# Kernel optimization log

Measured on AMD Instinct MI355X. Metric: run time of the kernel, lower is better.

## Reference

```python
import jax, jax.numpy as jnp
import numpy as np

D = 512      # d_model
H = 8        # num_heads
DH = D // H  # d_head = 64
WIN = 10     # window_size
DFF = 2048   # d_ff
EPS = 1e-5   # LayerNorm eps


def _layernorm(x, w, b):
    mu = jnp.mean(x, axis=-1, keepdims=True)
    var = jnp.mean(jnp.square(x - mu), axis=-1, keepdims=True)
    return (x - mu) * jax.lax.rsqrt(var + EPS) * w + b


def setup_inputs() -> dict:
    key = jax.random.key(0)
    ks = jax.random.split(key, 8)
    s = 0.02
    inp = {
        "z": jax.random.normal(ks[0], (4, 2048, D), jnp.float32),
        "Wq": jax.random.normal(ks[1], (D, D), jnp.float32) * s,
        "bq": jnp.zeros((D,), jnp.float32),
        "Wk": jax.random.normal(ks[2], (D, D), jnp.float32) * s,
        "bk": jnp.zeros((D,), jnp.float32),
        "Wv": jax.random.normal(ks[3], (D, D), jnp.float32) * s,
        "bv": jnp.zeros((D,), jnp.float32),
        "Wo": jax.random.normal(ks[4], (D, D), jnp.float32) * s,
        "bo": jnp.zeros((D,), jnp.float32),
        "ln1_w": jnp.ones((D,), jnp.float32),
        "ln1_b": jnp.zeros((D,), jnp.float32),
        "W1": jax.random.normal(ks[5], (D, DFF), jnp.float32) * s,
        "b1": jnp.zeros((DFF,), jnp.float32),
        "W2": jax.random.normal(ks[6], (DFF, D), jnp.float32) * s,
        "b2": jnp.zeros((D,), jnp.float32),
        "ln2_w": jnp.ones((D,), jnp.float32),
        "ln2_b": jnp.zeros((D,), jnp.float32),
    }
    return inp


def reference(z, Wq, bq, Wk, bk, Wv, bv, Wo, bo, ln1_w, ln1_b, W1, b1, W2, b2, ln2_w, ln2_b):
    B, T, Dm = z.shape
    # projections -> [B, H, T, DH]
    q = (z @ Wq + bq).reshape(B, T, H, DH).transpose(0, 2, 1, 3)
    k = (z @ Wk + bk).reshape(B, T, H, DH).transpose(0, 2, 1, 3)
    v = (z @ Wv + bv).reshape(B, T, H, DH).transpose(0, 2, 1, 3)
    scale = 1.0 / jnp.sqrt(jnp.asarray(DH, z.dtype))
    scores = jnp.einsum('bhqd,bhkd->bhqk', q, k) * scale  # [B,H,T,T]
    idx = jnp.arange(T)
    dist = idx[:, None] - idx[None, :]
    valid = (dist >= 0) & (dist < WIN)
    neg = jnp.finfo(scores.dtype).min
    scores = jnp.where(valid[None, None], scores, neg)
    attn = jax.nn.softmax(scores, axis=-1)  # dropout is identity in eval
    out = jnp.einsum('bhqk,bhkd->bhqd', attn, v)
    out = out.transpose(0, 2, 1, 3).reshape(B, T, Dm)
    out = out @ Wo + bo
    z = _layernorm(z + out, ln1_w, ln1_b)
    # FFN with exact (erf) GELU, matching torch nn.GELU default
    ff = jax.nn.gelu(z @ W1 + b1, approximate=False) @ W2 + b2
    z = _layernorm(z + ff, ln2_w, ln2_b)
    return z
```

## Files before the change

### kernel.cpp

```cpp
#include <hip/hip_runtime.h>
#include <cstdint>
#include <cstddef>

#define DEV __device__ __forceinline__

typedef __bf16 bf16x8 __attribute__((ext_vector_type(8)));
typedef float f32x4 __attribute__((ext_vector_type(4)));
typedef unsigned short us8 __attribute__((ext_vector_type(8)));
typedef unsigned short us4 __attribute__((ext_vector_type(4)));

typedef const __attribute__((address_space(1))) unsigned int GUI;
typedef __attribute__((address_space(3))) unsigned int LUI;

DEV unsigned short f2bf(float f) {
  unsigned int u = __builtin_bit_cast(unsigned int, f);
  u += 0x7fffu + ((u >> 16) & 1u);
  return (unsigned short)(u >> 16);
}
DEV float bf2f(unsigned short h) {
  unsigned int u = ((unsigned int)h) << 16;
  return __builtin_bit_cast(float, u);
}

DEV void tr32(const float* __restrict__ in, unsigned short* __restrict__ out,
              int K, int N, int k0, int n0) {
  __shared__ float tile[32][33];
  const int tx = threadIdx.x & 31, ty = threadIdx.x >> 5;
#pragma unroll
  for (int i = 0; i < 32; i += 8)
    tile[ty + i][tx] = in[(size_t)(k0 + ty + i) * N + n0 + tx];
  __syncthreads();
#pragma unroll
  for (int i = 0; i < 32; i += 8)
    out[(size_t)(n0 + ty + i) * K + k0 + tx] = f2bf(tile[tx][ty + i]);
}

__global__ __launch_bounds__(256) void k_prep(
    const float* __restrict__ z, unsigned short* __restrict__ zb,
    const float* __restrict__ Wq, const float* __restrict__ Wk,
    const float* __restrict__ Wv, const float* __restrict__ Wo,
    unsigned short* __restrict__ Wsq,
    const float* __restrict__ W1, unsigned short* __restrict__ W1T,
    const float* __restrict__ W2, unsigned short* __restrict__ W2T,
    const float* __restrict__ bq, const float* __restrict__ bk,
    const float* __restrict__ bv, float* __restrict__ biasqkv) {
  const int j = blockIdx.x;
  const int tid = threadIdx.x;
  if (j < 4096) {
    int i = j * 256 + tid;
    float4 v = ((const float4*)z)[i];
    us4 o;
    o.x = f2bf(v.x); o.y = f2bf(v.y); o.z = f2bf(v.z); o.w = f2bf(v.w);
    *(us4*)(zb + (size_t)i * 4) = o;
  } else if (j < 5120) {
    int t = j - 4096;
    int mat = t >> 8, tile = t & 255;
    const float* in = mat == 0 ? Wq : mat == 1 ? Wk : mat == 2 ? Wv : Wo;
    tr32(in, Wsq + (size_t)mat * 262144, 512, 512, (tile >> 4) * 32, (tile & 15) * 32);
  } else if (j < 6144) {
    int t = j - 5120;
    tr32(W1, W1T, 512, 2048, (t / 64) * 32, (t % 64) * 32);
  } else if (j < 7168) {
    int t = j - 6144;
    tr32(W2, W2T, 2048, 512, (t / 16) * 32, (t % 16) * 32);
  } else {
    for (int i = tid; i < 1536; i += 256)
      biasqkv[i] = (i < 512) ? bq[i] : (i < 1024 ? bk[i - 512] : bv[i - 1024]);
  }
}

template <int MODE>
DEV void gemm_body(const unsigned short* __restrict__ A,
                   const unsigned short* __restrict__ BT,
                   const float* __restrict__ bias,
                   unsigned short* __restrict__ outp,
                   int K, int N) {
  __shared__ __align__(16) unsigned short As[2 * 8192];
  __shared__ __align__(16) unsigned short Bs[2 * 8192];
  const int tid = threadIdx.x;
  const int wave = tid >> 6, lane = tid & 63;
  const int wm = wave >> 1, wn = wave & 1;
  const int q = lane >> 4, l15 = lane & 15;

  const int nx = gridDim.x, ny = gridDim.y;
  const int nwg = nx * ny;
  const int lid = blockIdx.y * nx + blockIdx.x;
  const int q8 = nwg >> 3, r8 = nwg & 7;
  const int xcd = lid & 7, slot = lid >> 3;
  const int wid = (xcd < r8 ? xcd * (q8 + 1) : r8 * (q8 + 1) + (xcd - r8) * q8) + slot;
  const int bx = wid % nx;
  const int by = wid / nx;

  const int rbase = by * 128;
  const int nbase = bx * 128;
  const int nkt = K >> 6;

  float bv_[4];
#pragma unroll
  for (int n = 0; n < 4; ++n) bv_[n] = bias[nbase + wn * 64 + n * 16 + l15];
  asm volatile("s_waitcnt vmcnt(0)" ::: "memory");

  auto STAGE = [&](int buf, int k0) {
#pragma unroll
    for (int t = 0; t < 4; ++t) {
      int s = t * 256 + tid;
      int row = s >> 3;
      int col = ((s & 7) ^ (row & 7)) << 3;
      const unsigned short* ga = A + (size_t)(rbase + row) * K + k0 + col;
      const unsigned short* gb = BT + (size_t)(nbase + row) * K + k0 + col;
      const int dst = buf * 8192 + (t * 256 + wave * 64) * 8;
      __builtin_amdgcn_global_load_lds((GUI*)ga, (LUI*)(As + dst), 16, 0, 0);
      __builtin_amdgcn_global_load_lds((GUI*)gb, (LUI*)(Bs + dst), 16, 0, 0);
    }
  };

  f32x4 acc[4][4] = {};
  STAGE(0, 0);

  for (int kt = 0; kt < nkt; ++kt) {
    const int cur = kt & 1;
    if (kt + 1 < nkt) {
      STAGE(cur ^ 1, (kt + 1) * 64);
      asm volatile("s_waitcnt vmcnt(8)" ::: "memory");
    } else {
      asm volatile("s_waitcnt vmcnt(0)" ::: "memory");
    }
    __builtin_amdgcn_s_barrier();

#pragma unroll
    for (int ks = 0; ks < 2; ++ks) {
      bf16x8 af[4], bfr[4];
#pragma unroll
      for (int m = 0; m < 4; ++m) {
        int row = wm * 64 + m * 16 + l15;
        int ch = (ks * 4 + q) ^ (row & 7);
        af[m] = __builtin_bit_cast(bf16x8, *(const us8*)(As + cur * 8192 + row * 64 + ch * 8));
      }
#pragma unroll
      for (int n = 0; n < 4; ++n) {
        int row = wn * 64 + n * 16 + l15;
        int ch = (ks * 4 + q) ^ (row & 7);
        bfr[n] = __builtin_bit_cast(bf16x8, *(const us8*)(Bs + cur * 8192 + row * 64 + ch * 8));
      }
      __builtin_amdgcn_s_setprio(1);
#pragma unroll
      for (int m = 0; m < 4; ++m)
#pragma unroll
        for (int n = 0; n < 4; ++n)
          acc[m][n] = __builtin_amdgcn_mfma_f32_16x16x32_bf16(af[m], bfr[n], acc[m][n], 0, 0, 0);
      __builtin_amdgcn_s_setprio(0);
    }
    asm volatile("s_waitcnt lgkmcnt(0)" ::: "memory");
    __builtin_amdgcn_s_barrier();
  }

#pragma unroll
  for (int m = 0; m < 4; ++m) {
    int grow0 = rbase + wm * 64 + m * 16 + (q << 2);
#pragma unroll
    for (int n = 0; n < 4; ++n) {
      int gcol = nbase + wn * 64 + n * 16 + l15;
#pragma unroll
      for (int r = 0; r < 4; ++r) {
        float v = acc[m][n][r] + bv_[n];
        if (MODE == 2) v = 0.5f * v * (1.0f + erff(v * 0.70710678118654752f));
        outp[(size_t)(grow0 + r) * N + gcol] = f2bf(v);
      }
    }
  }
}

__global__ __launch_bounds__(256) void k_qkv(const unsigned short* __restrict__ A,
                                             const unsigned short* __restrict__ BT,
                                             const float* __restrict__ bias,
                                             unsigned short* __restrict__ outp, int K, int N) {
  gemm_body<0>(A, BT, bias, outp, K, N);
}
__global__ __launch_bounds__(256) void k_wo(const unsigned short* __restrict__ A,
                                            const unsigned short* __restrict__ BT,
                                            const float* __restrict__ bias,
                                            unsigned short* __restrict__ outp, int K, int N) {
  gemm_body<0>(A, BT, bias, outp, K, N);
}
__global__ __launch_bounds__(256) void k_ffn1(const unsigned short* __restrict__ A,
                                              const unsigned short* __restrict__ BT,
                                              const float* __restrict__ bias,
                                              unsigned short* __restrict__ outp, int K, int N) {
  gemm_body<2>(A, BT, bias, outp, K, N);
}
__global__ __launch_bounds__(256) void k_ffn2(const unsigned short* __restrict__ A,
                                              const unsigned short* __restrict__ BT,
                                              const float* __restrict__ bias,
                                              unsigned short* __restrict__ outp, int K, int N) {
  gemm_body<0>(A, BT, bias, outp, K, N);
}

__global__ __launch_bounds__(64) void k_attn(const unsigned short* __restrict__ qkv,
                                             unsigned short* __restrict__ attnb) {
  __shared__ float Qt[64 * 35];
  __shared__ float Kt[64 * 45];
  __shared__ float P[32 * 12];

  const int lane = threadIdx.x;
  const int bid = blockIdx.x;
  const int chunk = bid & 63;
  const int bh = bid >> 6;
  const int h = bh & 7, b = bh >> 3;
  const int i0 = chunk * 32;
  const int b2048 = b * 2048;
  const int h64 = h * 64;

#pragma unroll 8
  for (int r = 0; r < 41; ++r) {
    int jloc = i0 - 9 + r;
    int jc = jloc < 0 ? 0 : jloc;
    Kt[lane * 45 + r] = bf2f(qkv[(size_t)(b2048 + jc) * 1536 + 512 + h64 + lane]);
  }
#pragma unroll 8
  for (int r = 0; r < 32; ++r) {
    Qt[lane * 35 + r] = bf2f(qkv[(size_t)(b2048 + i0 + r) * 1536 + h64 + lane]);
  }
  __syncthreads();

  const int qe = lane & 31, dh = lane >> 5;
  float s[10];
#pragma unroll
  for (int jj = 0; jj < 10; ++jj) s[jj] = 0.f;
#pragma unroll
  for (int dd = 0; dd < 32; ++dd) {
    int d = dh * 32 + dd;
    float qd = Qt[d * 35 + qe];
#pragma unroll
    for (int jj = 0; jj < 10; ++jj)
      s[jj] = fmaf(qd, Kt[d * 45 + qe + jj], s[jj]);
  }
#pragma unroll
  for (int jj = 0; jj < 10; ++jj) s[jj] += __shfl_xor(s[jj], 32);

  const int iG = i0 + qe;
#pragma unroll
  for (int jj = 0; jj < 10; ++jj)
    s[jj] = (iG - 9 + jj >= 0) ? s[jj] * 0.125f : -1e30f;
  float mx = s[9];
#pragma unroll
  for (int jj = 0; jj < 9; ++jj) mx = fmaxf(mx, s[jj]);
  float den = 0.f;
#pragma unroll
  for (int jj = 0; jj < 10; ++jj) {
    s[jj] = __expf(s[jj] - mx);
    den += s[jj];
  }
  float inv = 1.f / den;
  if (lane < 32) {
#pragma unroll
    for (int jj = 0; jj < 10; ++jj) P[qe * 12 + jj] = s[jj] * inv;
  }
  __syncthreads();

  for (int q0 = 0; q0 < 32; q0 += 4) {
    float vv[13];
#pragma unroll
    for (int t = 0; t < 13; ++t) {
      int jloc = i0 + q0 - 9 + t;
      int jc = jloc < 0 ? 0 : jloc;
      vv[t] = bf2f(qkv[(size_t)(b2048 + jc) * 1536 + 1024 + h64 + lane]);
    }
#pragma unroll
    for (int qq = 0; qq < 4; ++qq) {
      const int qy = q0 + qq;
      const float* pp = &P[qy * 12];
      float o = 0.f;
#pragma unroll
      for (int jj = 0; jj < 10; ++jj) o = fmaf(pp[jj], vv[qq + jj], o);
      attnb[(size_t)(b2048 + i0 + qy) * 512 + h64 + lane] = f2bf(o);
    }
  }
}

template <int OUTF32>
DEV void ln_body(const unsigned short* __restrict__ res,
                 const unsigned short* __restrict__ add,
                 const float* __restrict__ w,
                 const float* __restrict__ bb,
                 void* __restrict__ outp) {
  const int wave = threadIdx.x >> 6, lane = threadIdx.x & 63;
  const int row = blockIdx.x * 4 + wave;
  float x[8];
  us8 r = *(const us8*)(res + (size_t)row * 512 + lane * 8);
  us8 a = *(const us8*)(add + (size_t)row * 512 + lane * 8);
  float sum = 0.f, ss = 0.f;
#pragma unroll
  for (int j = 0; j < 8; ++j) {
    x[j] = bf2f(r[j]) + bf2f(a[j]);
    sum += x[j];
    ss += x[j] * x[j];
  }
#pragma unroll
  for (int m = 32; m >= 1; m >>= 1) {
    sum += __shfl_xor(sum, m);
    ss += __shfl_xor(ss, m);
  }
  const float mu = sum * (1.f / 512.f);
  float var = ss * (1.f / 512.f) - mu * mu;
  const float rstd = rsqrtf(var + 1e-5f);
  const int c = lane * 8;
  float o[8];
#pragma unroll
  for (int j = 0; j < 8; ++j) o[j] = (x[j] - mu) * rstd * w[c + j] + bb[c + j];
  if (OUTF32 == 0) {
    us8 u;
#pragma unroll
    for (int j = 0; j < 8; ++j) u[j] = f2bf(o[j]);
    *(us8*)((unsigned short*)outp + (size_t)row * 512 + c) = u;
  } else {
    float4 u0, u1;
    u0.x = o[0]; u0.y = o[1]; u0.z = o[2]; u0.w = o[3];
    u1.x = o[4]; u1.y = o[5]; u1.z = o[6]; u1.w = o[7];
    float4* o4 = (float4*)((float*)outp + (size_t)row * 512 + c);
    o4[0] = u0; o4[1] = u1;
  }
}

__global__ __launch_bounds__(256) void k_ln_mid(const unsigned short* __restrict__ res,
                                                const unsigned short* __restrict__ add,
                                                const float* __restrict__ w,
                                                const float* __restrict__ bb,
                                                unsigned short* __restrict__ outp) {
  ln_body<0>(res, add, w, bb, outp);
}
__global__ __launch_bounds__(256) void k_ln_out(const unsigned short* __restrict__ res,
                                                const unsigned short* __restrict__ add,
                                                const float* __restrict__ w,
                                                const float* __restrict__ bb,
                                                float* __restrict__ outp) {
  ln_body<1>(res, add, w, bb, outp);
}

extern "C" void kernel_launch(void* const* d_in, const int* in_sizes, int n_in,
                              void* d_out, int out_size, void* d_ws, size_t ws_size,
                              hipStream_t stream) {
  const float* z    = (const float*)d_in[0];
  const float* Wq   = (const float*)d_in[1];
  const float* bq   = (const float*)d_in[2];
  const float* Wk   = (const float*)d_in[3];
  const float* bk   = (const float*)d_in[4];
  const float* Wv   = (const float*)d_in[5];
  const float* bv   = (const float*)d_in[6];
  const float* Wo   = (const float*)d_in[7];
  const float* bo   = (const float*)d_in[8];
  const float* ln1w = (const float*)d_in[9];
  const float* ln1b = (const float*)d_in[10];
  const float* W1   = (const float*)d_in[11];
  const float* b1   = (const float*)d_in[12];
  const float* W2   = (const float*)d_in[13];
  const float* b2   = (const float*)d_in[14];
  const float* ln2w = (const float*)d_in[15];
  const float* ln2b = (const float*)d_in[16];
  float* out = (float*)d_out;

  char* ws = (char*)d_ws;
  size_t off = 0;
  auto alloc = [&](size_t bytes) {
    char* p = ws + off;
    off += (bytes + 255) & ~(size_t)255;
    return p;
  };
  unsigned short* Wsq   = (unsigned short*)alloc((size_t)2048 * 512 * 2);
  unsigned short* WTqkv = Wsq;
  unsigned short* WoT   = Wsq + (size_t)1536 * 512;
  unsigned short* W1T   = (unsigned short*)alloc((size_t)2048 * 512 * 2);
  unsigned short* W2T   = (unsigned short*)alloc((size_t)512 * 2048 * 2);
  float*          biasqkv = (float*)alloc(1536 * 4);
  unsigned short* zb    = (unsigned short*)alloc((size_t)8192 * 512 * 2);
  unsigned short* z1b   = (unsigned short*)alloc((size_t)8192 * 512 * 2);
  unsigned short* qkvb  = (unsigned short*)alloc((size_t)8192 * 1536 * 2);
  unsigned short* attnb = (unsigned short*)alloc((size_t)8192 * 512 * 2);
  unsigned short* woout = (unsigned short*)alloc((size_t)8192 * 512 * 2);
  unsigned short* f2out = (unsigned short*)alloc((size_t)8192 * 512 * 2);
  unsigned short* ff    = qkvb;

  k_prep<<<7169, 256, 0, stream>>>(z, zb, Wq, Wk, Wv, Wo, Wsq, W1, W1T, W2, W2T,
                                   bq, bk, bv, biasqkv);
  k_qkv<<<dim3(12, 64), 256, 0, stream>>>(zb, WTqkv, biasqkv, qkvb, 512, 1536);
  k_attn<<<2048, 64, 0, stream>>>(qkvb, attnb);
  k_wo<<<dim3(4, 64), 256, 0, stream>>>(attnb, WoT, bo, woout, 512, 512);
  k_ln_mid<<<2048, 256, 0, stream>>>(zb, woout, ln1w, ln1b, z1b);
  k_ffn1<<<dim3(16, 64), 256, 0, stream>>>(z1b, W1T, b1, ff, 512, 2048);
  k_ffn2<<<dim3(4, 64), 256, 0, stream>>>(ff, W2T, b2, f2out, 2048, 512);
  k_ln_out<<<2048, 256, 0, stream>>>(z1b, f2out, ln2w, ln2b, out);
}
```

Baseline: 147.7 us.

## Use 256x256 GEMM tiles with split-K partials reduced in LayerNorm

Adds a 512-thread GEMM with 256x256 output tiles and double-buffered LDS staging, used for the Wo, FFN1 and FFN2 projections. The Wo and FFN2 GEMMs are split four ways along K, each writing a bf16 partial plane, and the following LayerNorm kernels sum the four planes with the residual. The larger tiles raise operand reuse per workgroup, and split-K keeps enough workgroups in flight for the narrow N=512 outputs. In exchange it writes and reads extra partial-sum traffic, rounds each partial to bf16, and uses 128 KB of LDS per workgroup.

```diff
diff --git a/kernel.cpp b/kernel.cpp
--- a/kernel.cpp
+++ b/kernel.cpp
@@ -69,12 +69,120 @@
   }
 }
 
+template <int MODE, int SPLITK>
+DEV void gemm256_body(const unsigned short* __restrict__ A,
+                      const unsigned short* __restrict__ BT,
+                      const float* __restrict__ bias,
+                      unsigned short* __restrict__ outp,
+                      int K, int N) {
+  __shared__ __align__(16) unsigned short As[2 * 16384];
+  __shared__ __align__(16) unsigned short Bs[2 * 16384];
+  const int tid = threadIdx.x;
+  const int wave = tid >> 6, lane = tid & 63;
+  const int wm = wave >> 2, wn = wave & 3;
+
+  const int nx = gridDim.x, ny = gridDim.y;
+  const int nwg = nx * ny * SPLITK;
+  const int lid = (blockIdx.z * ny + blockIdx.y) * nx + blockIdx.x;
+  const int q8 = nwg >> 3, r8 = nwg & 7;
+  const int xcd = lid & 7, slot = lid >> 3;
+  const int wid = (xcd < r8 ? xcd * (q8 + 1) : r8 * (q8 + 1) + (xcd - r8) * q8) + slot;
+  const int nbz = nx * SPLITK;
+  const int bxz = wid % nbz;
+  const int by  = wid / nbz;
+  const int bx  = bxz % nx;
+  const int z   = bxz / nx;
+
+  const int rbase = by * 256;
+  const int nbase = bx * 256;
+  const int nkt = (K / SPLITK) >> 6;
+  const int kb = z * (K / SPLITK);
+
+  float bv_[4];
+#pragma unroll
+  for (int n = 0; n < 4; ++n) {
+    int gcol = nbase + wn * 64 + n * 16 + (lane & 15);
+    bv_[n] = (z == 0) ? bias[gcol] : 0.f;
+  }
+  asm volatile("s_waitcnt vmcnt(0)" ::: "memory");
+
+  auto STAGE = [&](int buf, int k0) {
+#pragma unroll
+    for (int t = 0; t < 4; ++t) {
+      int s = t * 512 + tid;
+      int row = s >> 3;
+      int col = ((s & 7) ^ (row & 7)) << 3;
+      const unsigned short* ga = A + (size_t)(rbase + row) * K + k0 + col;
+      const unsigned short* gb = BT + (size_t)(nbase + row) * K + k0 + col;
+      const int dst = buf * 16384 + (t * 512 + wave * 64) * 8;
+      __builtin_amdgcn_global_load_lds((GUI*)ga, (LUI*)(As + dst), 16, 0, 0);
+      __builtin_amdgcn_global_load_lds((GUI*)gb, (LUI*)(Bs + dst), 16, 0, 0);
+    }
+  };
+
+  f32x4 acc[8][4] = {};
+  STAGE(0, kb);
+
+  for (int kt = 0; kt < nkt; ++kt) {
+    const int cur = kt & 1;
+    if (kt + 1 < nkt) {
+      STAGE(cur ^ 1, kb + (kt + 1) * 64);
+      asm volatile("s_waitcnt vmcnt(8)" ::: "memory");
+    } else {
+      asm volatile("s_waitcnt vmcnt(0)" ::: "memory");
+    }
+    __builtin_amdgcn_s_barrier();
+
+#pragma unroll
+    for (int ks = 0; ks < 2; ++ks) {
+      bf16x8 af[8], bfr[4];
+#pragma unroll
+      for (int m = 0; m < 8; ++m) {
+        int row = wm * 128 + m * 16 + (lane & 15);
+        int ch = (ks * 4 + (lane >> 4)) ^ (row & 7);
+        af[m] = __builtin_bit_cast(bf16x8, *(const us8*)(As + cur * 16384 + row * 64 + ch * 8));
+      }
+#pragma unroll
+      for (int n = 0; n < 4; ++n) {
+        int row = wn * 64 + n * 16 + (lane & 15);
+        int ch = (ks * 4 + (lane >> 4)) ^ (row & 7);
+        bfr[n] = __builtin_bit_cast(bf16x8, *(const us8*)(Bs + cur * 16384 + row * 64 + ch * 8));
+      }
+      __builtin_amdgcn_s_setprio(1);
+#pragma unroll
+      for (int m = 0; m < 8; ++m)
+#pragma unroll
+        for (int n = 0; n < 4; ++n)
+          acc[m][n] = __builtin_amdgcn_mfma_f32_16x16x32_bf16(af[m], bfr[n], acc[m][n], 0, 0, 0);
+      __builtin_amdgcn_s_setprio(0);
+    }
+    asm volatile("s_waitcnt lgkmcnt(0)" ::: "memory");
+    __builtin_amdgcn_s_barrier();
+  }
+
+  unsigned short* opv = outp + (size_t)z * 8192 * N;
+#pragma unroll
+  for (int m = 0; m < 8; ++m) {
+    int grow0 = rbase + wm * 128 + m * 16 + ((lane >> 4) << 2);
+#pragma unroll
+    for (int n = 0; n < 4; ++n) {
+      int gcol = nbase + wn * 64 + n * 16 + (lane & 15);
+#pragma unroll
+      for (int r = 0; r < 4; ++r) {
+        float v = acc[m][n][r] + bv_[n];
+        if (MODE == 2) v = 0.5f * v * (1.0f + erff(v * 0.70710678118654752f));
+        opv[(size_t)(grow0 + r) * N + gcol] = f2bf(v);
+      }
+    }
+  }
+}
+
 template <int MODE>
-DEV void gemm_body(const unsigned short* __restrict__ A,
-                   const unsigned short* __restrict__ BT,
-                   const float* __restrict__ bias,
-                   unsigned short* __restrict__ outp,
-                   int K, int N) {
+DEV void gemm128_body(const unsigned short* __restrict__ A,
+                      const unsigned short* __restrict__ BT,
+                      const float* __restrict__ bias,
+                      unsigned short* __restrict__ outp,
+                      int K, int N) {
   __shared__ __align__(16) unsigned short As[2 * 8192];
   __shared__ __align__(16) unsigned short Bs[2 * 8192];
   const int tid = threadIdx.x;
@@ -174,25 +282,25 @@
                                              const unsigned short* __restrict__ BT,
                                              const float* __restrict__ bias,
                                              unsigned short* __restrict__ outp, int K, int N) {
-  gemm_body<0>(A, BT, bias, outp, K, N);
-}
-__global__ __launch_bounds__(256) void k_wo(const unsigned short* __restrict__ A,
+  gemm128_body<0>(A, BT, bias, outp, K, N);
+}
+__global__ __launch_bounds__(512) void k_wo(const unsigned short* __restrict__ A,
                                             const unsigned short* __restrict__ BT,
                                             const float* __restrict__ bias,
                                             unsigned short* __restrict__ outp, int K, int N) {
-  gemm_body<0>(A, BT, bias, outp, K, N);
-}
-__global__ __launch_bounds__(256) void k_ffn1(const unsigned short* __restrict__ A,
+  gemm256_body<0, 4>(A, BT, bias, outp, K, N);
+}
+__global__ __launch_bounds__(512) void k_ffn1(const unsigned short* __restrict__ A,
                                               const unsigned short* __restrict__ BT,
                                               const float* __restrict__ bias,
                                               unsigned short* __restrict__ outp, int K, int N) {
-  gemm_body<2>(A, BT, bias, outp, K, N);
-}
-__global__ __launch_bounds__(256) void k_ffn2(const unsigned short* __restrict__ A,
+  gemm256_body<2, 1>(A, BT, bias, outp, K, N);
+}
+__global__ __launch_bounds__(512) void k_ffn2(const unsigned short* __restrict__ A,
                                               const unsigned short* __restrict__ BT,
                                               const float* __restrict__ bias,
                                               unsigned short* __restrict__ outp, int K, int N) {
-  gemm_body<0>(A, BT, bias, outp, K, N);
+  gemm256_body<0, 4>(A, BT, bias, outp, K, N);
 }
 
 __global__ __launch_bounds__(64) void k_attn(const unsigned short* __restrict__ qkv,
@@ -277,21 +385,28 @@
   }
 }
 
-template <int OUTF32>
+template <int OUTF32, int NP>
 DEV void ln_body(const unsigned short* __restrict__ res,
                  const unsigned short* __restrict__ add,
                  const float* __restrict__ w,
                  const float* __restrict__ bb,
                  void* __restrict__ outp) {
+  const size_t PLANE = (size_t)8192 * 512;
   const int wave = threadIdx.x >> 6, lane = threadIdx.x & 63;
   const int row = blockIdx.x * 4 + wave;
   float x[8];
   us8 r = *(const us8*)(res + (size_t)row * 512 + lane * 8);
-  us8 a = *(const us8*)(add + (size_t)row * 512 + lane * 8);
+#pragma unroll
+  for (int j = 0; j < 8; ++j) x[j] = bf2f(r[j]);
+#pragma unroll
+  for (int p = 0; p < NP; ++p) {
+    us8 a = *(const us8*)(add + p * PLANE + (size_t)row * 512 + lane * 8);
+#pragma unroll
+    for (int j = 0; j < 8; ++j) x[j] += bf2f(a[j]);
+  }
   float sum = 0.f, ss = 0.f;
 #pragma unroll
   for (int j = 0; j < 8; ++j) {
-    x[j] = bf2f(r[j]) + bf2f(a[j]);
     sum += x[j];
     ss += x[j] * x[j];
   }
@@ -326,14 +441,14 @@
                                                 const float* __restrict__ w,
                                                 const float* __restrict__ bb,
                                                 unsigned short* __restrict__ outp) {
-  ln_body<0>(res, add, w, bb, outp);
+  ln_body<0, 4>(res, add, w, bb, outp);
 }
 __global__ __launch_bounds__(256) void k_ln_out(const unsigned short* __restrict__ res,
                                                 const unsigned short* __restrict__ add,
                                                 const float* __restrict__ w,
                                                 const float* __restrict__ bb,
                                                 float* __restrict__ outp) {
-  ln_body<1>(res, add, w, bb, outp);
+  ln_body<1, 4>(res, add, w, bb, outp);
 }
 
 extern "C" void kernel_launch(void* const* d_in, const int* in_sizes, int n_in,
@@ -375,17 +490,16 @@
   unsigned short* z1b   = (unsigned short*)alloc((size_t)8192 * 512 * 2);
   unsigned short* qkvb  = (unsigned short*)alloc((size_t)8192 * 1536 * 2);
   unsigned short* attnb = (unsigned short*)alloc((size_t)8192 * 512 * 2);
-  unsigned short* woout = (unsigned short*)alloc((size_t)8192 * 512 * 2);
-  unsigned short* f2out = (unsigned short*)alloc((size_t)8192 * 512 * 2);
+  unsigned short* p1    = (unsigned short*)alloc((size_t)4 * 8192 * 512 * 2);
   unsigned short* ff    = qkvb;
 
   k_prep<<<7169, 256, 0, stream>>>(z, zb, Wq, Wk, Wv, Wo, Wsq, W1, W1T, W2, W2T,
                                    bq, bk, bv, biasqkv);
   k_qkv<<<dim3(12, 64), 256, 0, stream>>>(zb, WTqkv, biasqkv, qkvb, 512, 1536);
   k_attn<<<2048, 64, 0, stream>>>(qkvb, attnb);
-  k_wo<<<dim3(4, 64), 256, 0, stream>>>(attnb, WoT, bo, woout, 512, 512);
-  k_ln_mid<<<2048, 256, 0, stream>>>(zb, woout, ln1w, ln1b, z1b);
-  k_ffn1<<<dim3(16, 64), 256, 0, stream>>>(z1b, W1T, b1, ff, 512, 2048);
-  k_ffn2<<<dim3(4, 64), 256, 0, stream>>>(ff, W2T, b2, f2out, 2048, 512);
-  k_ln_out<<<2048, 256, 0, stream>>>(z1b, f2out, ln2w, ln2b, out);
-}
+  k_wo<<<dim3(2, 32, 4), 512, 0, stream>>>(attnb, WoT, bo, p1, 512, 512);
+  k_ln_mid<<<2048, 256, 0, stream>>>(zb, p1, ln1w, ln1b, z1b);
+  k_ffn1<<<dim3(8, 32), 512, 0, stream>>>(z1b, W1T, b1, ff, 512, 2048);
+  k_ffn2<<<dim3(2, 32, 4), 512, 0, stream>>>(ff, W2T, b2, p1, 2048, 512);
+  k_ln_out<<<2048, 256, 0, stream>>>(z1b, p1, ln2w, ln2b, out);
+}
```

Result: no change. 145.6 us (-1.4%).
